# Optimization experiments

Measured on AMD Instinct MI355X. Metric: run time of the kernel, lower is better.

Reference implementation:

```python
import jax, jax.numpy as jnp
import numpy as np

EMA_PERIOD = 25
LOOKBACK = 25
UPPER = 15.0
LOWER = -15.0
ADJUST = True


def setup_inputs() -> dict:
    key = jax.random.key(0)
    x = jax.random.normal(key, (64, 4096, 64), dtype=jnp.float32)
    return {"x": x}


def _ema(x):
    # x: [B, T, F]. Recurrence: e_t = alpha*x_t + (1-alpha)*e_{t-1},
    # then (adjust) divided by bias-correction weight 1-(1-alpha)^(t+1),
    # where the *corrected* value is carried forward (faithful to source).
    alpha = jnp.asarray(2.0 / (EMA_PERIOD + 1.0), dtype=x.dtype)
    om = jnp.asarray(1.0, dtype=x.dtype) - alpha
    T = x.shape[1]
    ema0 = x[:, 0, :]                       # [B, F]
    xs = jnp.swapaxes(x[:, 1:, :], 0, 1)    # [T-1, B, F]
    tp1 = jnp.arange(2, T + 1, dtype=x.dtype)  # exponent t+1 for t=1..T-1

    def step(carry, inp):
        xt, e_exp = inp
        e = alpha * xt + om * carry
        if ADJUST:
            w = 1.0 - om ** e_exp
            e = e / jnp.maximum(w, 1e-10)
        return e, e

    _, rest = jax.lax.scan(step, ema0, (xs, tp1))  # rest: [T-1, B, F]
    return jnp.concatenate([ema0[:, None, :], jnp.swapaxes(rest, 0, 1)], axis=1)


def reference(x):
    ema = _ema(x)  # [B, T, F]
    L = LOOKBOOK if False else LOOKBACK
    # lagged EMA: zeros for first L steps, EMA_{t-L} after
    lagged = jnp.pad(ema[:, :-L, :], ((0, 0), (L, 0), (0, 0)))
    slope = ema - lagged
    one = jnp.asarray(1.0, dtype=x.dtype)
    zero = jnp.asarray(0.0, dtype=x.dtype)
    signal_above = jnp.where(slope > UPPER, one, zero)
    signal_below = jnp.where(slope < LOWER, one, zero)
    signal_between = jnp.where((slope >= LOWER) & (slope <= UPPER), one, zero)
    return (ema, slope, signal_above, signal_below, signal_between)
```

## Files before the change

kernel.cpp:

```cpp
#include <hip/hip_runtime.h>


constexpr int kB  = 64;
constexpr int kT  = 4096;
constexpr int kF  = 64;
constexpr int kNC = 32;
constexpr int kC  = kT / kNC;
constexpr int kW  = 256;
constexpr int kLag = 25;
constexpr float kUpper = 15.0f;
constexpr float kLower = -15.0f;
constexpr size_t kN = (size_t)kB * kT * kF;

__global__ __launch_bounds__(256)
void ema_slope_kernel(const float* __restrict__ x, float* __restrict__ out) {
    const float kAlpha = (float)(2.0 / 26.0);
    const float kOm    = 1.0f - kAlpha;

    __shared__ float s_w[256];
    __shared__ float s_ring[256 * kLag];

    {
        const int t = threadIdx.x;
        const double omd = (double)kOm;
        double p = 1.0;
        for (int i = 0; i <= t; ++i) p *= omd;
        s_w[t] = fmaxf(1.0f - (float)p, 1e-10f);
    }
    __syncthreads();

    const int lane  = threadIdx.x & 63;
    const int wv    = threadIdx.x >> 6;
    const int chunk = blockIdx.x % kNC;
    const int b     = (blockIdx.x / kNC) * 4 + wv;

    const int t_out0 = chunk * kC;
    const int t_end  = t_out0 + kC;
    const int tl0    = t_end - (kC + kW);

    const float* xb = x   + (size_t)b * kT * kF + lane;
    float*       o0 = out + (size_t)b * kT * kF + lane;

    float* ring = &s_ring[(size_t)threadIdx.x * kLag];

    float c;
    if (tl0 <= 0) {
        c = xb[0];
        ring[0] = c;
        if (chunk == 0) {
            float slope = c;
            o0[0]      = c;
            o0[kN]     = slope;
            o0[2 * kN] = (slope > kUpper) ? 1.0f : 0.0f;
            o0[3 * kN] = (slope < kLower) ? 1.0f : 0.0f;
            o0[4 * kN] = (slope >= kLower && slope <= kUpper) ? 1.0f : 0.0f;
        }
    } else {
        c = 0.0f;
    }

    constexpr int G = 16;
    float xpre[G];
#pragma unroll
    for (int j = 0; j < G; ++j) {
        int tj = tl0 + j;
        float v = 0.0f;
        if (tj >= 0) v = xb[(size_t)tj * kF];
        xpre[j] = v;
    }

    const int ngroups = (kC + kW) / G;
    for (int g = 0; g < ngroups; ++g) {
        const int tg = tl0 + g * G;
        float xnext[G];
        if (g + 1 < ngroups) {
#pragma unroll
            for (int j = 0; j < G; ++j) {
                int tj = tg + G + j;
                float v = 0.0f;
                if (tj >= 0) v = xb[(size_t)tj * kF];
                xnext[j] = v;
            }
        }
#pragma unroll
        for (int j = 0; j < G; ++j) {
            const int tj = tg + j;
            if (tj >= 1) {
                float e = __fadd_rn(__fmul_rn(kAlpha, xpre[j]), __fmul_rn(kOm, c));
                c = (tj < 256) ? __fdiv_rn(e, s_w[tj]) : e;

                const int slot = (unsigned)tj % (unsigned)kLag;
                float lagv = ring[slot];
                ring[slot] = c;

                if (tj >= t_out0) {
                    float slope = (tj >= kLag) ? __fsub_rn(c, lagv) : c;
                    size_t off = (size_t)tj * kF;
                    o0[off]          = c;
                    o0[off + kN]     = slope;
                    o0[off + 2 * kN] = (slope > kUpper) ? 1.0f : 0.0f;
                    o0[off + 3 * kN] = (slope < kLower) ? 1.0f : 0.0f;
                    o0[off + 4 * kN] = (slope >= kLower && slope <= kUpper) ? 1.0f : 0.0f;
                }
            }
        }
        if (g + 1 < ngroups) {
#pragma unroll
            for (int j = 0; j < G; ++j) xpre[j] = xnext[j];
        }
    }
}

extern "C" void kernel_launch(void* const* d_in, const int* in_sizes, int n_in,
                              void* d_out, int out_size, void* d_ws, size_t ws_size,
                              hipStream_t stream) {
    const float* x = (const float*)d_in[0];
    float* out = (float*)d_out;
    dim3 grid(kB / 4 * kNC);
    dim3 block(256);
    ema_slope_kernel<<<grid, block, 0, stream>>>(x, out);
}
```

Baseline: 404.2 us.

## Stage EMA rows in a per-wave LDS window and emit float4 output stores

Replaces the per-thread modulo-25 ring buffer with a per-wave shared-memory window of 64 time rows. Inside the recurrence loop each lane now only writes its EMA value into the window. After each 16-step group, the wave reads the window back in a transposed pattern, computes slope against the row 25 steps earlier, and writes all five outputs with 16-byte float4 stores. This removes the per-step modulo, the ring traffic and the scalar stores from the serial loop. The cost is extra LDS writes and reads, and it relies on intra-wave LDS visibility with no barrier between them.

Result: no change. 401.8 us (-0.6%).

```diff
diff --git a/kernel.cpp b/kernel.cpp
--- a/kernel.cpp
+++ b/kernel.cpp
@@ -8,6 +8,7 @@
 constexpr int kC  = kT / kNC;
 constexpr int kW  = 256;
 constexpr int kLag = 25;
+constexpr int kWin = 64;
 constexpr float kUpper = 15.0f;
 constexpr float kLower = -15.0f;
 constexpr size_t kN = (size_t)kB * kT * kF;
@@ -18,7 +19,7 @@
     const float kOm    = 1.0f - kAlpha;
 
     __shared__ float s_w[256];
-    __shared__ float s_ring[256 * kLag];
+    __shared__ float s_win[4][kWin][kF];
 
     {
         const int t = threadIdx.x;
@@ -39,22 +40,14 @@
     const int tl0    = t_end - (kC + kW);
 
     const float* xb = x   + (size_t)b * kT * kF + lane;
-    float*       o0 = out + (size_t)b * kT * kF + lane;
+    float*       o0 = out + (size_t)b * kT * kF;
 
-    float* ring = &s_ring[(size_t)threadIdx.x * kLag];
+    float (*win)[kF] = s_win[wv];
 
     float c;
     if (tl0 <= 0) {
         c = xb[0];
-        ring[0] = c;
-        if (chunk == 0) {
-            float slope = c;
-            o0[0]      = c;
-            o0[kN]     = slope;
-            o0[2 * kN] = (slope > kUpper) ? 1.0f : 0.0f;
-            o0[3 * kN] = (slope < kLower) ? 1.0f : 0.0f;
-            o0[4 * kN] = (slope >= kLower && slope <= kUpper) ? 1.0f : 0.0f;
-        }
+        win[0][lane] = c;
     } else {
         c = 0.0f;
     }
@@ -64,10 +57,11 @@
 #pragma unroll
     for (int j = 0; j < G; ++j) {
         int tj = tl0 + j;
-        float v = 0.0f;
-        if (tj >= 0) v = xb[(size_t)tj * kF];
-        xpre[j] = v;
+        xpre[j] = (tj >= 0) ? xb[(size_t)tj * kF] : 0.0f;
     }
+
+    const int rsub = lane >> 4;
+    const int colf = (lane & 15) * 4;
 
     const int ngroups = (kC + kW) / G;
     for (int g = 0; g < ngroups; ++g) {
@@ -77,33 +71,59 @@
 #pragma unroll
             for (int j = 0; j < G; ++j) {
                 int tj = tg + G + j;
-                float v = 0.0f;
-                if (tj >= 0) v = xb[(size_t)tj * kF];
-                xnext[j] = v;
+                xnext[j] = (tj >= 0) ? xb[(size_t)tj * kF] : 0.0f;
             }
         }
+
+        const bool needw = (tg + G) > (t_out0 - kLag);
+
 #pragma unroll
         for (int j = 0; j < G; ++j) {
             const int tj = tg + j;
             if (tj >= 1) {
                 float e = __fadd_rn(__fmul_rn(kAlpha, xpre[j]), __fmul_rn(kOm, c));
-                c = (tj < 256) ? __fdiv_rn(e, s_w[tj]) : e;
-
-                const int slot = (unsigned)tj % (unsigned)kLag;
-                float lagv = ring[slot];
-                ring[slot] = c;
-
-                if (tj >= t_out0) {
-                    float slope = (tj >= kLag) ? __fsub_rn(c, lagv) : c;
-                    size_t off = (size_t)tj * kF;
-                    o0[off]          = c;
-                    o0[off + kN]     = slope;
-                    o0[off + 2 * kN] = (slope > kUpper) ? 1.0f : 0.0f;
-                    o0[off + 3 * kN] = (slope < kLower) ? 1.0f : 0.0f;
-                    o0[off + 4 * kN] = (slope >= kLower && slope <= kUpper) ? 1.0f : 0.0f;
-                }
+                if (tj < 256) e = __fdiv_rn(e, s_w[tj]);
+                c = e;
+                if (needw) win[tj & (kWin - 1)][lane] = c;
             }
         }
+
+        if (tg >= t_out0) {
+#pragma unroll
+            for (int r4 = 0; r4 < 4; ++r4) {
+                const int row = tg + r4 * 4 + rsub;
+                const float4 ema4 = *(const float4*)&win[row & (kWin - 1)][colf];
+                const float4 lraw = *(const float4*)&win[(row - kLag) & (kWin - 1)][colf];
+
+                float4 sl;
+                sl.x = (row >= kLag) ? __fsub_rn(ema4.x, lraw.x) : ema4.x;
+                sl.y = (row >= kLag) ? __fsub_rn(ema4.y, lraw.y) : ema4.y;
+                sl.z = (row >= kLag) ? __fsub_rn(ema4.z, lraw.z) : ema4.z;
+                sl.w = (row >= kLag) ? __fsub_rn(ema4.w, lraw.w) : ema4.w;
+
+                float4 sa, sb, sc;
+                sa.x = (sl.x > kUpper) ? 1.0f : 0.0f;
+                sa.y = (sl.y > kUpper) ? 1.0f : 0.0f;
+                sa.z = (sl.z > kUpper) ? 1.0f : 0.0f;
+                sa.w = (sl.w > kUpper) ? 1.0f : 0.0f;
+                sb.x = (sl.x < kLower) ? 1.0f : 0.0f;
+                sb.y = (sl.y < kLower) ? 1.0f : 0.0f;
+                sb.z = (sl.z < kLower) ? 1.0f : 0.0f;
+                sb.w = (sl.w < kLower) ? 1.0f : 0.0f;
+                sc.x = (sl.x >= kLower && sl.x <= kUpper) ? 1.0f : 0.0f;
+                sc.y = (sl.y >= kLower && sl.y <= kUpper) ? 1.0f : 0.0f;
+                sc.z = (sl.z >= kLower && sl.z <= kUpper) ? 1.0f : 0.0f;
+                sc.w = (sl.w >= kLower && sl.w <= kUpper) ? 1.0f : 0.0f;
+
+                float* p = o0 + (size_t)(tg + r4 * 4) * kF + lane * 4;
+                *(float4*)(p)          = ema4;
+                *(float4*)(p + kN)     = sl;
+                *(float4*)(p + 2 * kN) = sa;
+                *(float4*)(p + 3 * kN) = sb;
+                *(float4*)(p + 4 * kN) = sc;
+            }
+        }
+
         if (g + 1 < ngroups) {
 #pragma unroll
             for (int j = 0; j < G; ++j) xpre[j] = xnext[j];
```
